# Kernel tuning notes

Hardware: AMD Instinct MI355X
Metric: run time of the kernel (lower is better)

The kernel has to match this reference:

```python
import jax, jax.numpy as jnp
import numpy as np

CHEBYSHEV_K = 5  # number of Chebyshev polynomial terms


def setup_inputs() -> dict:
    key = jax.random.key(0)
    k1, k2, k3 = jax.random.split(key, 3)
    B, N, F_in, F_out = 1024, 512, 16, 8
    x = jax.random.normal(k1, (B, N, F_in), dtype=jnp.float32)
    # symmetric scaled-Laplacian-like matrix, scaled small so recurrence stays stable
    A = jax.random.normal(k2, (N, N), dtype=jnp.float32) / jnp.sqrt(jnp.float32(N))
    L = 0.5 * (A + A.T)
    # xavier-uniform-like weights [K, F_in, F_out]
    limit = np.sqrt(6.0 / (F_in + F_out)).astype(np.float32)
    W = jax.random.uniform(k3, (CHEBYSHEV_K, F_in, F_out), dtype=jnp.float32,
                           minval=-limit, maxval=limit)
    b = jnp.zeros((F_out,), dtype=jnp.float32)
    return {"x": x, "L": L, "W": W, "b": b}


def reference(x, L, W, b):
    # x: [B, N, F_in], L: [N, N], W: [K, F_in, F_out], b: [F_out]
    Lx = lambda z: jnp.einsum('nm,bmf->bnf', L, z)
    Z0 = x
    Z1 = Lx(x)
    out = Z0 @ W[0] + Z1 @ W[1]
    for k in range(2, CHEBYSHEV_K):  # small fixed K, structural loop
        Zk = 2.0 * Lx(Z1) - Z0
        out = out + Zk @ W[k]
        Z0, Z1 = Z1, Zk
    return out + b
```

## Files before the change

kernel.cpp:

```cpp
#include <hip/hip_runtime.h>
#include <cstdint>
#include <cstddef>


typedef __attribute__((ext_vector_type(8))) short  frag_ab;
typedef __attribute__((ext_vector_type(4))) float  frag_cd;

constexpr int BN    = 512;
constexpr int FIN   = 16;
constexpr int FOUT  = 8;
constexpr int BT    = 4;
constexpr int NCOLS = BT * FIN;
constexpr int LDST  = BN + 8;
constexpr int ZBUF  = NCOLS * LDST;

__device__ __forceinline__ uint16_t f2bf(float f) {
    uint32_t u = __builtin_bit_cast(uint32_t, f);
    u += 0x7FFFu + ((u >> 16) & 1u);
    return (uint16_t)(u >> 16);
}
__device__ __forceinline__ float bf2f(uint16_t h) {
    uint32_t u = ((uint32_t)h) << 16;
    return __builtin_bit_cast(float, u);
}

__global__ void cvtL(const float* __restrict__ Lf, uint16_t* __restrict__ Lb) {
    int i = blockIdx.x * 256 + threadIdx.x;
    Lb[i] = f2bf(Lf[i]);
}

template <bool LBF16>
__global__ __launch_bounds__(512, 2)
void cheb_kernel(const float* __restrict__ x, const float* __restrict__ Lf,
                 const uint16_t* __restrict__ Lb, const float* __restrict__ W,
                 const float* __restrict__ bvec, float* __restrict__ out) {
    __shared__ uint16_t lds[2 * ZBUF];
    uint16_t* z0 = lds;
    uint16_t* z1 = lds + ZBUF;

    const int tid  = threadIdx.x;
    const int wave = tid >> 6;
    const int lane = tid & 63;
    const int lr   = lane & 15;
    const int q    = lane >> 4;

    const float4* x4 = reinterpret_cast<const float4*>(x + (size_t)blockIdx.x * (BT * BN * FIN));
    for (int s = 0; s < 2; ++s) {
        int a   = tid + s * 512;
        int f0g = a & 3;
        int n8  = (a >> 2) & 63;
        int bl  = a >> 8;
        int jb  = bl * 2048 + n8 * 32 + f0g;
        float4 v[8];
#pragma unroll
        for (int r = 0; r < 8; ++r) v[r] = x4[jb + r * 4];
        int cb = bl * 16 + f0g * 4;
        int nb = n8 * 8;
#pragma unroll
        for (int w = 0; w < 4; ++w) {
            frag_ab pk;
#pragma unroll
            for (int r = 0; r < 8; ++r)
                pk[r] = (short)f2bf(reinterpret_cast<const float*>(&v[r])[w]);
            *reinterpret_cast<frag_ab*>(&z0[(cb + w) * LDST + nb]) = pk;
        }
    }

    frag_ab wf[3];
#pragma unroll
    for (int p = 0; p < 3; ++p) {
        frag_ab t;
#pragma unroll
        for (int jj = 0; jj < 8; ++jj) {
            int k   = q * 8 + jj;
            int ki  = p * 2 + (k >> 4);
            int fin = k & 15;
            float val = (lr < 8 && ki < 5) ? W[ki * (FIN * FOUT) + fin * FOUT + lr] : 0.0f;
            t[jj] = (short)f2bf(val);
        }
        wf[p] = t;
    }
    const float bv = (lr < 8) ? bvec[lr] : 0.0f;

    frag_cd accOut[4][4] = {};

    auto loadA = [&](int mt, int ks) -> frag_ab {
        int row = mt * 16 + lr;
        int kb  = ks * 32 + q * 8;
        if constexpr (LBF16) {
            return *reinterpret_cast<const frag_ab*>(Lb + row * BN + kb);
        } else {
            const float4* p  = reinterpret_cast<const float4*>(Lf + row * BN + kb);
            float4 u0 = p[0], u1 = p[1];
            frag_ab t;
            t[0] = (short)f2bf(u0.x); t[1] = (short)f2bf(u0.y);
            t[2] = (short)f2bf(u0.z); t[3] = (short)f2bf(u0.w);
            t[4] = (short)f2bf(u1.x); t[5] = (short)f2bf(u1.y);
            t[6] = (short)f2bf(u1.z); t[7] = (short)f2bf(u1.w);
            return t;
        }
    };

    auto app = [&](const uint16_t* cur, uint16_t* dst, bool first) {
        frag_cd acc[4][4] = {};
        for (int ks = 0; ks < 16; ++ks) {
            frag_ab bfr[4];
#pragma unroll
            for (int ct = 0; ct < 4; ++ct)
                bfr[ct] = *reinterpret_cast<const frag_ab*>(
                    cur + (ct * 16 + lr) * LDST + ks * 32 + q * 8);
#pragma unroll
            for (int mi = 0; mi < 4; ++mi) {
                frag_ab a = loadA(wave + mi * 8, ks);
#pragma unroll
                for (int ct = 0; ct < 4; ++ct)
                    acc[mi][ct] = __builtin_amdgcn_mfma_f32_16x16x32_bf16(
                        a, bfr[ct], acc[mi][ct], 0, 0, 0);
            }
        }
#pragma unroll
        for (int mi = 0; mi < 4; ++mi) {
            int row0 = (wave + mi * 8) * 16 + q * 4;
#pragma unroll
            for (int ct = 0; ct < 4; ++ct) {
                uint16_t* dp = dst + (ct * 16 + lr) * LDST + row0;
                float pz[4] = {0.f, 0.f, 0.f, 0.f};
                if (!first) {
                    ushort4 pv = *reinterpret_cast<const ushort4*>(dp);
                    pz[0] = bf2f(pv.x); pz[1] = bf2f(pv.y);
                    pz[2] = bf2f(pv.z); pz[3] = bf2f(pv.w);
                }
                ushort4 nv;
                float v0 = acc[mi][ct][0], v1 = acc[mi][ct][1];
                float v2 = acc[mi][ct][2], v3 = acc[mi][ct][3];
                if (!first) {
                    v0 = 2.f * v0 - pz[0]; v1 = 2.f * v1 - pz[1];
                    v2 = 2.f * v2 - pz[2]; v3 = 2.f * v3 - pz[3];
                }
                nv.x = f2bf(v0); nv.y = f2bf(v1); nv.z = f2bf(v2); nv.w = f2bf(v3);
                *reinterpret_cast<ushort4*>(dp) = nv;
            }
        }
    };

    auto epi = [&](const uint16_t* bA, const uint16_t* bB, frag_ab wfr) {
        const uint16_t* base = (q < 2) ? bA : bB;
        int finb = (q & 1) * 8;
#pragma unroll
        for (int mi = 0; mi < 4; ++mi) {
            int n = (wave + mi * 8) * 16 + lr;
#pragma unroll
            for (int bt = 0; bt < 4; ++bt) {
                const uint16_t* pp = base + (bt * 16 + finb) * LDST + n;
                frag_ab afr;
#pragma unroll
                for (int jj = 0; jj < 8; ++jj) afr[jj] = (short)pp[jj * LDST];
                accOut[mi][bt] = __builtin_amdgcn_mfma_f32_16x16x32_bf16(
                    afr, wfr, accOut[mi][bt], 0, 0, 0);
            }
        }
    };

    __syncthreads();
    app(z0, z1, true);
    __syncthreads();
    epi(z0, z1, wf[0]);
    __syncthreads();
    app(z1, z0, false);
    __syncthreads();
    app(z0, z1, false);
    __syncthreads();
    epi(z0, z1, wf[1]);
    __syncthreads();
    app(z1, z0, false);
    __syncthreads();
    epi(z0, z0, wf[2]);

    if (lr < 8) {
        float* ob = out + (size_t)blockIdx.x * BT * BN * FOUT;
#pragma unroll
        for (int mi = 0; mi < 4; ++mi) {
            int row0 = (wave + mi * 8) * 16 + q * 4;
#pragma unroll
            for (int bt = 0; bt < 4; ++bt) {
                float* op = ob + bt * (BN * FOUT) + row0 * FOUT + lr;
                op[0 * FOUT] = accOut[mi][bt][0] + bv;
                op[1 * FOUT] = accOut[mi][bt][1] + bv;
                op[2 * FOUT] = accOut[mi][bt][2] + bv;
                op[3 * FOUT] = accOut[mi][bt][3] + bv;
            }
        }
    }
}

extern "C" void kernel_launch(void* const* d_in, const int* in_sizes, int n_in,
                              void* d_out, int out_size, void* d_ws, size_t ws_size,
                              hipStream_t stream) {
    const float* x  = (const float*)d_in[0];
    const float* Lf = (const float*)d_in[1];
    const float* W  = (const float*)d_in[2];
    const float* bv = (const float*)d_in[3];
    float* out = (float*)d_out;

    if (ws_size >= (size_t)(BN * BN * sizeof(uint16_t))) {
        uint16_t* Lb = (uint16_t*)d_ws;
        cvtL<<<dim3(1024), dim3(256), 0, stream>>>(Lf, Lb);
        cheb_kernel<true><<<dim3(256), dim3(512), 0, stream>>>(x, Lf, Lb, W, bv, out);
    } else {
        cheb_kernel<false><<<dim3(256), dim3(512), 0, stream>>>(x, Lf, nullptr, W, bv, out);
    }
}
```

Measured before the change: 156.5 us.

## Precompute 2L²−I and apply L and M together to halve recurrence depth

Adds a kernel that computes M = 2L²−I in bf16 using a split-precision MFMA, then runs the Chebyshev recurrence in two rounds. Each round multiplies the current block by both L and M at once, so the fifth term comes from one product. The subtracted Z0 and Z1 terms are folded into combined weights W0−W4 and W1−W3. This cuts serialized stages and barriers and reuses LDS B fragments across two matrices. In exchange it adds an extra launch and extra global reads of M, and rounding M to bf16 adds error.

```diff
diff --git a/kernel.cpp b/kernel.cpp
--- a/kernel.cpp
+++ b/kernel.cpp
@@ -29,11 +29,215 @@
     Lb[i] = f2bf(Lf[i]);
 }
 
+__global__ __launch_bounds__(256)
+void m2comp(const float* __restrict__ Lf, uint16_t* __restrict__ Mb) {
+    const int tid = threadIdx.x;
+    const int wv = tid >> 6, lane = tid & 63, lr = lane & 15, q = lane >> 4;
+    const int i0 = (blockIdx.x >> 4) * 32 + (wv >> 1) * 16;
+    const int j0 = (blockIdx.x & 15) * 32 + (wv & 1) * 16;
+    frag_cd acc = {0.f, 0.f, 0.f, 0.f};
+    const float* arow = Lf + (size_t)(i0 + lr) * BN;
+    const float* brow = Lf + (size_t)(j0 + lr) * BN;
+    for (int ks = 0; ks < 16; ++ks) {
+        const int kb = ks * 32 + q * 8;
+        const float4* ap = reinterpret_cast<const float4*>(arow + kb);
+        const float4* bp = reinterpret_cast<const float4*>(brow + kb);
+        float4 a0 = ap[0], a1 = ap[1], b0 = bp[0], b1 = bp[1];
+        float av[8]  = {a0.x, a0.y, a0.z, a0.w, a1.x, a1.y, a1.z, a1.w};
+        float bvv[8] = {b0.x, b0.y, b0.z, b0.w, b1.x, b1.y, b1.z, b1.w};
+        frag_ab ah, al, bh, bl;
+#pragma unroll
+        for (int j = 0; j < 8; ++j) {
+            uint16_t h = f2bf(av[j]);
+            ah[j] = (short)h;
+            al[j] = (short)f2bf(av[j] - bf2f(h));
+            uint16_t g = f2bf(bvv[j]);
+            bh[j] = (short)g;
+            bl[j] = (short)f2bf(bvv[j] - bf2f(g));
+        }
+        acc = __builtin_amdgcn_mfma_f32_16x16x32_bf16(ah, bh, acc, 0, 0, 0);
+        acc = __builtin_amdgcn_mfma_f32_16x16x32_bf16(ah, bl, acc, 0, 0, 0);
+        acc = __builtin_amdgcn_mfma_f32_16x16x32_bf16(al, bh, acc, 0, 0, 0);
+    }
+#pragma unroll
+    for (int r = 0; r < 4; ++r) {
+        int i = i0 + q * 4 + r, j = j0 + lr;
+        float v = 2.f * acc[r] - ((i == j) ? 1.f : 0.f);
+        Mb[(size_t)i * BN + j] = f2bf(v);
+    }
+}
+
+__global__ __launch_bounds__(512, 2)
+void cheb2_kernel(const float* __restrict__ x, const uint16_t* __restrict__ Lb,
+                  const uint16_t* __restrict__ Mb, const float* __restrict__ W,
+                  const float* __restrict__ bvec, float* __restrict__ out) {
+    __shared__ uint16_t lds[2 * ZBUF];
+    uint16_t* z0 = lds;
+    uint16_t* z1 = lds + ZBUF;
+
+    const int tid  = threadIdx.x;
+    const int wave = tid >> 6;
+    const int lane = tid & 63;
+    const int lr   = lane & 15;
+    const int q    = lane >> 4;
+
+    const float4* x4 = reinterpret_cast<const float4*>(x + (size_t)blockIdx.x * (BT * BN * FIN));
+    for (int s = 0; s < 2; ++s) {
+        int a   = tid + s * 512;
+        int f0g = a & 3;
+        int n8  = (a >> 2) & 63;
+        int bl  = a >> 8;
+        int jb  = bl * 2048 + n8 * 32 + f0g;
+        float4 v[8];
+#pragma unroll
+        for (int r = 0; r < 8; ++r) v[r] = x4[jb + r * 4];
+        int cb = bl * 16 + f0g * 4;
+        int nb = n8 * 8;
+#pragma unroll
+        for (int w = 0; w < 4; ++w) {
+            frag_ab pk;
+#pragma unroll
+            for (int r = 0; r < 8; ++r)
+                pk[r] = (short)f2bf(reinterpret_cast<const float*>(&v[r])[w]);
+            *reinterpret_cast<frag_ab*>(&z0[(cb + w) * LDST + nb]) = pk;
+        }
+    }
+
+    frag_ab wf[3];
+#pragma unroll
+    for (int p = 0; p < 3; ++p) {
+        frag_ab t;
+#pragma unroll
+        for (int jj = 0; jj < 8; ++jj) {
+            int k   = q * 8 + jj;
+            int ki  = p * 2 + (k >> 4);
+            int fin = k & 15;
+            float val = 0.0f;
+            if (lr < 8) {
+                int idx = fin * FOUT + lr;
+                if      (ki == 0) val = W[idx] - W[4 * (FIN * FOUT) + idx];
+                else if (ki == 1) val = W[1 * (FIN * FOUT) + idx] - W[3 * (FIN * FOUT) + idx];
+                else if (ki < 5)  val = W[ki * (FIN * FOUT) + idx];
+            }
+            t[jj] = (short)f2bf(val);
+        }
+        wf[p] = t;
+    }
+    const float bv = (lr < 8) ? bvec[lr] : 0.0f;
+
+    frag_cd accOut[4][4] = {};
+
+    auto loadA = [&](const uint16_t* M, int mt, int ks) -> frag_ab {
+        return *reinterpret_cast<const frag_ab*>(M + (size_t)(mt * 16 + lr) * BN + ks * 32 + q * 8);
+    };
+
+    frag_cd acc1[4][4];
+    frag_cd acc2[4][4];
+
+    auto round = [&](const uint16_t* cur) {
+#pragma unroll
+        for (int mi = 0; mi < 4; ++mi)
+#pragma unroll
+            for (int ct = 0; ct < 4; ++ct) {
+                acc1[mi][ct] = (frag_cd){0.f, 0.f, 0.f, 0.f};
+                acc2[mi][ct] = (frag_cd){0.f, 0.f, 0.f, 0.f};
+            }
+        for (int ks = 0; ks < 16; ++ks) {
+            frag_ab bfr[4];
+#pragma unroll
+            for (int ct = 0; ct < 4; ++ct)
+                bfr[ct] = *reinterpret_cast<const frag_ab*>(
+                    cur + (ct * 16 + lr) * LDST + ks * 32 + q * 8);
+#pragma unroll
+            for (int mi = 0; mi < 4; ++mi) {
+                frag_ab a = loadA(Lb, wave + mi * 8, ks);
+                frag_ab m = loadA(Mb, wave + mi * 8, ks);
+#pragma unroll
+                for (int ct = 0; ct < 4; ++ct)
+                    acc1[mi][ct] = __builtin_amdgcn_mfma_f32_16x16x32_bf16(
+                        a, bfr[ct], acc1[mi][ct], 0, 0, 0);
+#pragma unroll
+                for (int ct = 0; ct < 4; ++ct)
+                    acc2[mi][ct] = __builtin_amdgcn_mfma_f32_16x16x32_bf16(
+                        m, bfr[ct], acc2[mi][ct], 0, 0, 0);
+            }
+        }
+    };
+
+    auto wb = [&](frag_cd (&acc)[4][4], uint16_t* dst, float scale) {
+#pragma unroll
+        for (int mi = 0; mi < 4; ++mi) {
+            int row0 = (wave + mi * 8) * 16 + q * 4;
+#pragma unroll
+            for (int ct = 0; ct < 4; ++ct) {
+                uint16_t* dp = dst + (ct * 16 + lr) * LDST + row0;
+                ushort4 nv;
+                nv.x = f2bf(scale * acc[mi][ct][0]);
+                nv.y = f2bf(scale * acc[mi][ct][1]);
+                nv.z = f2bf(scale * acc[mi][ct][2]);
+                nv.w = f2bf(scale * acc[mi][ct][3]);
+                *reinterpret_cast<ushort4*>(dp) = nv;
+            }
+        }
+    };
+
+    auto epi = [&](const uint16_t* bA, const uint16_t* bB, frag_ab wfr) {
+        const uint16_t* base = (q < 2) ? bA : bB;
+        int finb = (q & 1) * 8;
+#pragma unroll
+        for (int mi = 0; mi < 4; ++mi) {
+            int n = (wave + mi * 8) * 16 + lr;
+#pragma unroll
+            for (int bt = 0; bt < 4; ++bt) {
+                const uint16_t* pp = base + (bt * 16 + finb) * LDST + n;
+                frag_ab afr;
+#pragma unroll
+                for (int jj = 0; jj < 8; ++jj) afr[jj] = (short)pp[jj * LDST];
+                accOut[mi][bt] = __builtin_amdgcn_mfma_f32_16x16x32_bf16(
+                    afr, wfr, accOut[mi][bt], 0, 0, 0);
+            }
+        }
+    };
+
+    __syncthreads();
+    round(z0);
+    wb(acc1, z1, 1.f);
+    __syncthreads();
+    epi(z0, z1, wf[0]);
+    __syncthreads();
+    wb(acc2, z0, 1.f);
+    __syncthreads();
+    round(z0);
+    wb(acc1, z1, 2.f);
+    __syncthreads();
+    epi(z0, z1, wf[1]);
+    __syncthreads();
+    wb(acc2, z0, 2.f);
+    __syncthreads();
+    epi(z0, z0, wf[2]);
+
+    if (lr < 8) {
+        float* ob = out + (size_t)blockIdx.x * BT * BN * FOUT;
+#pragma unroll
+        for (int mi = 0; mi < 4; ++mi) {
+            int row0 = (wave + mi * 8) * 16 + q * 4;
+#pragma unroll
+            for (int bt = 0; bt < 4; ++bt) {
+                float* op = ob + bt * (BN * FOUT) + row0 * FOUT + lr;
+                op[0 * FOUT] = accOut[mi][bt][0] + bv;
+                op[1 * FOUT] = accOut[mi][bt][1] + bv;
+                op[2 * FOUT] = accOut[mi][bt][2] + bv;
+                op[3 * FOUT] = accOut[mi][bt][3] + bv;
+            }
+        }
+    }
+}
+
 template <bool LBF16>
 __global__ __launch_bounds__(512, 2)
-void cheb_kernel(const float* __restrict__ x, const float* __restrict__ Lf,
-                 const uint16_t* __restrict__ Lb, const float* __restrict__ W,
-                 const float* __restrict__ bvec, float* __restrict__ out) {
+void cheb1_kernel(const float* __restrict__ x, const float* __restrict__ Lf,
+                  const uint16_t* __restrict__ Lb, const float* __restrict__ W,
+                  const float* __restrict__ bvec, float* __restrict__ out) {
     __shared__ uint16_t lds[2 * ZBUF];
     uint16_t* z0 = lds;
     uint16_t* z1 = lds + ZBUF;
@@ -202,11 +406,19 @@
     const float* bv = (const float*)d_in[3];
     float* out = (float*)d_out;
 
-    if (ws_size >= (size_t)(BN * BN * sizeof(uint16_t))) {
+    const size_t matB = (size_t)BN * BN * sizeof(uint16_t);
+
+    if (ws_size >= 2 * matB) {
+        uint16_t* Lb = (uint16_t*)d_ws;
+        uint16_t* Mb = Lb + (size_t)BN * BN;
+        cvtL<<<dim3(1024), dim3(256), 0, stream>>>(Lf, Lb);
+        m2comp<<<dim3(256), dim3(256), 0, stream>>>(Lf, Mb);
+        cheb2_kernel<<<dim3(256), dim3(512), 0, stream>>>(x, Lb, Mb, W, bv, out);
+    } else if (ws_size >= matB) {
         uint16_t* Lb = (uint16_t*)d_ws;
         cvtL<<<dim3(1024), dim3(256), 0, stream>>>(Lf, Lb);
-        cheb_kernel<true><<<dim3(256), dim3(512), 0, stream>>>(x, Lf, Lb, W, bv, out);
+        cheb1_kernel<true><<<dim3(256), dim3(512), 0, stream>>>(x, Lf, Lb, W, bv, out);
     } else {
-        cheb_kernel<false><<<dim3(256), dim3(512), 0, stream>>>(x, Lf, nullptr, W, bv, out);
-    }
-}
+        cheb1_kernel<false><<<dim3(256), dim3(512), 0, stream>>>(x, Lf, nullptr, W, bv, out);
+    }
+}
```

New measurement: 174.4 us. +11.4%, slower.
